# Kernel optimization log

Hardware: AMD Instinct MI355X
Metric: run time of the kernel (lower is better)

## Reference

```python
import jax, jax.numpy as jnp
import numpy as np
import math

LN_EPS = 1e-5

def layer_norm(x, g, b):
    m = x.mean(-1, keepdims=True)
    v = ((x - m) ** 2).mean(-1, keepdims=True)
    return (x - m) / jnp.sqrt(v + LN_EPS) * g + b

def bchw_to_bhwc(x):
    N, C, H, W = x.shape
    return x.transpose(0, 2, 3, 1).reshape(N, H * W, C)

def attw_matmul(weight, feature):
    # weight: [N,Q,K], feature: [N,C,FH,FW]; H=sqrt(Q), W=sqrt(K)
    N, Q, K = weight.shape
    _, C, FH, FW = feature.shape
    H, W = int(math.sqrt(Q)), int(math.sqrt(K))
    sH, sW = FH // H, FW // W
    # einsum('nij,ncjq->nciq', w, f).sum(3) == einsum over block-summed feature
    fs = feature.reshape(N, C, H, sH, W, sW).sum(axis=(3, 5)).reshape(N, C, H * W)  # [N,C,HW]
    r = jnp.einsum('nik,nck->nci', weight, fs)  # [N,C,HW]
    # broadcast-repeat each coarse cell back to its sH x sW block
    r = jnp.broadcast_to(r.reshape(N, C, H, 1, W, 1), (N, C, H, sH, W, sW))
    return r.reshape(N, C, H * sH, W * sW)

def reference(weight, feature, ln1_g, ln1_b, W1, b1, W2, b2, ln2_g, ln2_b, original_shape):
    residual = bchw_to_bhwc(feature)               # [N, FH*FW, C]
    x = bchw_to_bhwc(attw_matmul(weight, feature)) # [N, FH*FW, C]
    x = layer_norm(residual + x, ln1_g, ln1_b)
    residual = x
    h = jax.nn.gelu(x @ W1.T + b1, approximate=False)  # [N, T, dff]
    x = h @ W2.T + b2
    x = layer_norm(residual + x, ln2_g, ln2_b)
    return x

def setup_inputs() -> dict:
    key = jax.random.key(0)
    ks = jax.random.split(key, 8)
    N, C, FH, FW = 8, 256, 80, 80
    Q = K = 400
    hid, dff = 256, 1024
    s1 = 1.0 / math.sqrt(hid)
    s2 = 1.0 / math.sqrt(dff)
    return {
        "weight": jax.random.normal(ks[0], (N, Q, K), jnp.float32),
        "feature": jax.random.normal(ks[1], (N, C, FH, FW), jnp.float32),
        "ln1_g": jnp.ones((hid,), jnp.float32),
        "ln1_b": jnp.zeros((hid,), jnp.float32),
        "W1": jax.random.uniform(ks[2], (dff, hid), jnp.float32, -s1, s1),
        "b1": jax.random.uniform(ks[3], (dff,), jnp.float32, -s1, s1),
        "W2": jax.random.uniform(ks[4], (hid, dff), jnp.float32, -s2, s2),
        "b2": jax.random.uniform(ks[5], (hid,), jnp.float32, -s2, s2),
        "ln2_g": jnp.ones((hid,), jnp.float32),
        "ln2_b": jnp.zeros((hid,), jnp.float32),
        "original_shape": 80,
    }
```

## Files before the change

### kernel.cpp

```cpp
#include <hip/hip_runtime.h>
#include <hip/hip_bf16.h>
#include <math.h>

#define LN_EPS 1e-5f

typedef __attribute__((ext_vector_type(4))) float f4_t;
typedef __attribute__((ext_vector_type(8))) short bf8_t;

__device__ __forceinline__ unsigned short f2bf(float x) {
    unsigned u = __builtin_bit_cast(unsigned, x);
    unsigned r = (u + 0x7FFFu + ((u >> 16) & 1u)) >> 16;
    return (unsigned short)r;
}
__device__ __forceinline__ float bf2f(unsigned short u) {
    return __builtin_bit_cast(float, ((unsigned)u) << 16);
}
__device__ __forceinline__ float gelu_f(float x) {
    float z = x * 0.70710678f;
    float az = fabsf(z);
    float t = __builtin_amdgcn_rcpf(1.f + 0.3275911f * az);
    float y = t * (0.254829592f + t * (-0.284496736f + t * (1.421413741f +
              t * (-1.453152027f + t * 1.061405429f))));
    float e = 1.f - y * __expf(-az * az);
    return 0.5f * x * (1.f + copysignf(e, x));
}

__device__ __forceinline__ void light_barrier() {
    asm volatile("s_waitcnt lgkmcnt(0)" ::: "memory");
    __builtin_amdgcn_s_barrier();
}

__global__ __launch_bounds__(256) void pool_cvt_kernel(
    const float* __restrict__ feature, float* __restrict__ fs,
    const float* __restrict__ W1, const float* __restrict__ W2,
    bf8_t* __restrict__ W1f, bf8_t* __restrict__ W2f) {
    __shared__ float ftile[6400];
    int tid = threadIdx.x;
    if (blockIdx.x >= 2048) {
        int gid = (blockIdx.x - 2048) * 256 + tid;
        union { bf8_t v; unsigned short u[8]; } pk;
        if (gid < 32768) {
            int lane = gid & 63;
            int f = (gid >> 9) * 16 + (lane & 15);
            int k = ((gid >> 6) & 7) * 32 + (lane >> 4) * 8;
            const float* src = W1 + (size_t)f * 256 + k;
#pragma unroll
            for (int e = 0; e < 8; ++e) pk.u[e] = f2bf(src[e]);
            W1f[gid] = pk.v;
        } else {
            int g = gid - 32768;
            int lane = g & 63;
            int c = (g >> 11) * 16 + (lane & 15);
            int k = ((g >> 6) & 31) * 32 + (lane >> 4) * 8;
            const float* src = W2 + (size_t)c * 1024 + k;
#pragma unroll
            for (int e = 0; e < 8; ++e) pk.u[e] = f2bf(src[e]);
            W2f[g] = pk.v;
        }
        return;
    }
    int b = blockIdx.x;
    int n = b >> 8, c = b & 255;
    const float4* src = reinterpret_cast<const float4*>(feature + ((size_t)b) * 6400);
#pragma unroll
    for (int i = 0; i < 6; ++i) {
        int idx = i * 256 + tid;
        float4 v = src[idx];
        *reinterpret_cast<float4*>(&ftile[idx * 4]) = v;
    }
    if (tid < 64) {
        int idx = 1536 + tid;
        float4 v = src[idx];
        *reinterpret_cast<float4*>(&ftile[idx * 4]) = v;
    }
    __syncthreads();
    float* dst = fs + (size_t)n * 400 * 256 + c;
#pragma unroll
    for (int pass = 0; pass < 2; ++pass) {
        int k = pass * 256 + tid;
        if (k < 400) {
            int h = k / 20, w = k % 20;
            const float* p = &ftile[(h * 4) * 80 + w * 4];
            float s = 0.f;
#pragma unroll
            for (int dh = 0; dh < 4; ++dh)
                s += p[dh * 80 + 0] + p[dh * 80 + 1] + p[dh * 80 + 2] + p[dh * 80 + 3];
            dst[(size_t)k * 256] = s;
        }
    }
}

__global__ __launch_bounds__(256) void att_kernel(const float* __restrict__ wgt,
                                                  const float* __restrict__ fs,
                                                  float* __restrict__ r) {
    __shared__ float fsl[64][256];
    __shared__ float wl[8][64];
    int b = blockIdx.x;
    int n = b / 50, i0 = (b % 50) * 8;
    int tid = threadIdx.x;
    const float* wbase = wgt + (size_t)n * 400 * 400;
    const float* fsbase = fs + (size_t)n * 400 * 256;
    float acc[8] = {0.f, 0.f, 0.f, 0.f, 0.f, 0.f, 0.f, 0.f};
    for (int k0 = 0; k0 < 400; k0 += 64) {
        int kn = (k0 + 64 <= 400) ? 64 : (400 - k0);
        for (int kk = 0; kk < kn; ++kk)
            fsl[kk][tid] = fsbase[(size_t)(k0 + kk) * 256 + tid];
#pragma unroll
        for (int pass = 0; pass < 2; ++pass) {
            int idx = pass * 256 + tid;
            int ii = idx >> 6, kk = idx & 63;
            if (kk < kn)
                wl[ii][kk] = wbase[(size_t)(i0 + ii) * 400 + k0 + kk];
        }
        __syncthreads();
        for (int kk = 0; kk < kn; ++kk) {
            float f = fsl[kk][tid];
#pragma unroll
            for (int ii = 0; ii < 8; ++ii) acc[ii] += wl[ii][kk] * f;
        }
        __syncthreads();
    }
#pragma unroll
    for (int ii = 0; ii < 8; ++ii)
        r[((size_t)n * 400 + i0 + ii) * 256 + tid] = acc[ii];
}

__global__ __launch_bounds__(256, 2) void main_kernel(
    const float* __restrict__ feat, const float* __restrict__ r,
    const float* __restrict__ ln1g, const float* __restrict__ ln1b,
    const bf8_t* __restrict__ W1f, const float* __restrict__ b1,
    const bf8_t* __restrict__ W2f, const float* __restrict__ b2,
    const float* __restrict__ ln2g, const float* __restrict__ ln2b,
    float* __restrict__ out) {
    __shared__ unsigned short xt[64 * 256];
    __shared__ unsigned short ht[2][32 * 128];
    __shared__ float psum[4][64], psq[4][64];
    __shared__ float stat[2][64];

    int bid = blockIdx.x;
    int n = bid / 100;
    int p0 = (bid % 100) * 64;
    int tid = threadIdx.x;
    int lane = tid & 63;
    int q = tid >> 6;
    int t = lane;
    int p = p0 + t;
    int iatt = ((p / 80) >> 2) * 20 + ((p % 80) >> 2);

    const float* fbase = feat + ((size_t)(n * 256 + q * 64)) * 6400 + p;
    const float* rrow = r + ((size_t)(n * 400 + iatt)) * 256 + q * 64;
    float s1 = 0.f, s2 = 0.f;
#pragma unroll
    for (int jj = 0; jj < 8; ++jj) {
        union { bf8_t v; unsigned short u[8]; } pk;
#pragma unroll
        for (int e = 0; e < 8; ++e) {
            int j = jj * 8 + e;
            float v = fbase[(size_t)j * 6400] + rrow[j];
            s1 += v;
            s2 += v * v;
            pk.u[e] = f2bf(v);
        }
        int byte = t * 512 + ((q * 128 + jj * 16) ^ ((t & 7) << 4));
        *reinterpret_cast<bf8_t*>(reinterpret_cast<char*>(xt) + byte) = pk.v;
    }
    psum[q][t] = s1;
    psq[q][t] = s2;
    light_barrier();
    if (tid < 64) {
        float a = psum[0][tid] + psum[1][tid] + psum[2][tid] + psum[3][tid];
        float b = psq[0][tid] + psq[1][tid] + psq[2][tid] + psq[3][tid];
        float mu = a * (1.f / 256.f);
        float var = b * (1.f / 256.f) - mu * mu;
        stat[0][tid] = mu;
        stat[1][tid] = rsqrtf(var + LN_EPS);
    }
    light_barrier();
    float mu = stat[0][t], rs = stat[1][t];
#pragma unroll
    for (int jj = 0; jj < 8; ++jj) {
        int byte = t * 512 + ((q * 128 + jj * 16) ^ ((t & 7) << 4));
        union { bf8_t v; unsigned short u[8]; } pk;
        pk.v = *reinterpret_cast<const bf8_t*>(reinterpret_cast<const char*>(xt) + byte);
#pragma unroll
        for (int e = 0; e < 8; ++e) {
            int c = q * 64 + jj * 8 + e;
            float v = bf2f(pk.u[e]);
            pk.u[e] = f2bf((v - mu) * rs * ln1g[c] + ln1b[c]);
        }
        *reinterpret_cast<bf8_t*>(reinterpret_cast<char*>(xt) + byte) = pk.v;
    }
    light_barrier();

    int lm = lane & 15, lk = lane >> 4;
    const char* xtb = reinterpret_cast<const char*>(xt);

    f4_t oacc[16];
#pragma unroll
    for (int i = 0; i < 16; ++i) oacc[i] = (f4_t){0.f, 0.f, 0.f, 0.f};

    bf8_t bfr0[8];
    {
        const bf8_t* w1p = W1f + ((size_t)(0 * 8 + 2 * q) * 8) * 64 + lane;
#pragma unroll
        for (int kb = 0; kb < 4; ++kb) {
            bfr0[kb * 2 + 0] = w1p[(0 * 8 + kb) * 64];
            bfr0[kb * 2 + 1] = w1p[(1 * 8 + kb) * 64];
        }
    }

    for (int fc = 0; fc < 8; ++fc) {
        const bf8_t* w1p = W1f + ((size_t)(fc * 8 + 2 * q) * 8) * 64 + lane;
        f4_t hacc[8];
#pragma unroll
        for (int i = 0; i < 8; ++i) hacc[i] = (f4_t){0.f, 0.f, 0.f, 0.f};
#pragma unroll
        for (int kbh = 0; kbh < 2; ++kbh) {
            bf8_t bfr[8];
            if (kbh == 0) {
#pragma unroll
                for (int i = 0; i < 8; ++i) bfr[i] = bfr0[i];
            } else {
#pragma unroll
                for (int kb = 0; kb < 4; ++kb) {
                    bfr[kb * 2 + 0] = w1p[(0 * 8 + 4 + kb) * 64];
                    bfr[kb * 2 + 1] = w1p[(1 * 8 + 4 + kb) * 64];
                }
            }
#pragma unroll
            for (int kb = 0; kb < 4; ++kb) {
                int kbb = kbh * 4 + kb;
#pragma unroll
                for (int hh = 0; hh < 2; ++hh) {
#pragma unroll
                    for (int m = 0; m < 2; ++m) {
                        int row = hh * 32 + m * 16 + lm;
                        bf8_t a = *reinterpret_cast<const bf8_t*>(
                            xtb + row * 512 + ((kbb * 64 + lk * 16) ^ ((row & 7) << 4)));
                        hacc[hh * 4 + m * 2 + 0] = __builtin_amdgcn_mfma_f32_16x16x32_bf16(a, bfr[kb * 2 + 0], hacc[hh * 4 + m * 2 + 0], 0, 0, 0);
                        hacc[hh * 4 + m * 2 + 1] = __builtin_amdgcn_mfma_f32_16x16x32_bf16(a, bfr[kb * 2 + 1], hacc[hh * 4 + m * 2 + 1], 0, 0, 0);
                    }
                }
            }
        }
        const bf8_t* w2p = W2f + ((size_t)(q * 4) * 32 + fc * 4) * 64 + lane;
        bf8_t b2rA[8];
#pragma unroll
        for (int kb = 0; kb < 4; ++kb) {
            b2rA[kb * 2 + 0] = w2p[(0 * 32 + kb) * 64];
            b2rA[kb * 2 + 1] = w2p[(1 * 32 + kb) * 64];
        }
#pragma unroll
        for (int hh = 0; hh < 2; ++hh) {
            char* htc = reinterpret_cast<char*>(ht[hh]);
#pragma unroll
            for (int ftl = 0; ftl < 2; ++ftl) {
                int fl = (2 * q + ftl) * 16 + lm;
                float bias = b1[fc * 128 + fl];
#pragma unroll
                for (int m = 0; m < 2; ++m) {
#pragma unroll
                    for (int j = 0; j < 4; ++j) {
                        int row = m * 16 + lk * 4 + j;
                        float gv = gelu_f(hacc[hh * 4 + m * 2 + ftl][j] + bias);
                        *reinterpret_cast<unsigned short*>(
                            htc + row * 256 + ((fl * 2) ^ ((row & 7) << 4))) = f2bf(gv);
                    }
                }
            }
        }
        light_barrier();
        bf8_t b2rB[8];
#pragma unroll
        for (int kb = 0; kb < 4; ++kb) {
            b2rB[kb * 2 + 0] = w2p[(2 * 32 + kb) * 64];
            b2rB[kb * 2 + 1] = w2p[(3 * 32 + kb) * 64];
        }
        if (fc < 7) {
            const bf8_t* w1n = W1f + ((size_t)((fc + 1) * 8 + 2 * q) * 8) * 64 + lane;
#pragma unroll
            for (int kb = 0; kb < 4; ++kb) {
                bfr0[kb * 2 + 0] = w1n[(0 * 8 + kb) * 64];
                bfr0[kb * 2 + 1] = w1n[(1 * 8 + kb) * 64];
            }
        }
#pragma unroll
        for (int hh = 0; hh < 2; ++hh) {
            const char* htc = reinterpret_cast<const char*>(ht[hh]);
#pragma unroll
            for (int kb = 0; kb < 4; ++kb) {
#pragma unroll
                for (int m = 0; m < 2; ++m) {
                    int row = m * 16 + lm;
                    bf8_t a = *reinterpret_cast<const bf8_t*>(
                        htc + row * 256 + ((kb * 64 + lk * 16) ^ ((row & 7) << 4)));
                    oacc[hh * 8 + m * 4 + 0] = __builtin_amdgcn_mfma_f32_16x16x32_bf16(a, b2rA[kb * 2 + 0], oacc[hh * 8 + m * 4 + 0], 0, 0, 0);
                    oacc[hh * 8 + m * 4 + 1] = __builtin_amdgcn_mfma_f32_16x16x32_bf16(a, b2rA[kb * 2 + 1], oacc[hh * 8 + m * 4 + 1], 0, 0, 0);
                    oacc[hh * 8 + m * 4 + 2] = __builtin_amdgcn_mfma_f32_16x16x32_bf16(a, b2rB[kb * 2 + 0], oacc[hh * 8 + m * 4 + 2], 0, 0, 0);
                    oacc[hh * 8 + m * 4 + 3] = __builtin_amdgcn_mfma_f32_16x16x32_bf16(a, b2rB[kb * 2 + 1], oacc[hh * 8 + m * 4 + 3], 0, 0, 0);
                }
            }
        }
        light_barrier();
    }

    float b2l[4];
#pragma unroll
    for (int cl = 0; cl < 4; ++cl) b2l[cl] = b2[(q * 4 + cl) * 16 + lm];
#pragma unroll
    for (int hh = 0; hh < 2; ++hh) {
#pragma unroll
        for (int m = 0; m < 2; ++m) {
#pragma unroll
            for (int j = 0; j < 4; ++j) {
                int row = hh * 32 + m * 16 + lk * 4 + j;
                float s = 0.f, ss = 0.f;
#pragma unroll
                for (int cl = 0; cl < 4; ++cl) {
                    int c = (q * 4 + cl) * 16 + lm;
                    float res = bf2f(*reinterpret_cast<const unsigned short*>(
                        xtb + row * 512 + ((c * 2) ^ ((row & 7) << 4))));
                    float v = oacc[hh * 8 + m * 4 + cl][j] + b2l[cl] + res;
                    oacc[hh * 8 + m * 4 + cl][j] = v;
                    s += v;
                    ss += v * v;
                }
#pragma unroll
                for (int d = 1; d < 16; d <<= 1) {
                    s += __shfl_xor(s, d, 64);
                    ss += __shfl_xor(ss, d, 64);
                }
                if (lm == 0) { psum[q][row] = s; psq[q][row] = ss; }
            }
        }
    }
    light_barrier();
    if (tid < 64) {
        float a = psum[0][tid] + psum[1][tid] + psum[2][tid] + psum[3][tid];
        float b = psq[0][tid] + psq[1][tid] + psq[2][tid] + psq[3][tid];
        float mu2 = a * (1.f / 256.f);
        float var = b * (1.f / 256.f) - mu2 * mu2;
        stat[0][tid] = mu2;
        stat[1][tid] = rsqrtf(var + LN_EPS);
    }
    light_barrier();
    float g2[4], be2[4];
#pragma unroll
    for (int cl = 0; cl < 4; ++cl) {
        int c = (q * 4 + cl) * 16 + lm;
        g2[cl] = ln2g[c];
        be2[cl] = ln2b[c];
    }
    float* obase = out + ((size_t)(n * 6400 + p0)) * 256;
#pragma unroll
    for (int hh = 0; hh < 2; ++hh) {
#pragma unroll
        for (int m = 0; m < 2; ++m) {
#pragma unroll
            for (int j = 0; j < 4; ++j) {
                int row = hh * 32 + m * 16 + lk * 4 + j;
                float mu2 = stat[0][row], r2 = stat[1][row];
#pragma unroll
                for (int cl = 0; cl < 4; ++cl) {
                    int c = (q * 4 + cl) * 16 + lm;
                    obase[(size_t)row * 256 + c] =
                        (oacc[hh * 8 + m * 4 + cl][j] - mu2) * r2 * g2[cl] + be2[cl];
                }
            }
        }
    }
}

extern "C" void kernel_launch(void* const* d_in, const int* in_sizes, int n_in,
                              void* d_out, int out_size, void* d_ws, size_t ws_size,
                              hipStream_t stream) {
    const float* weight = (const float*)d_in[0];
    const float* feature = (const float*)d_in[1];
    const float* ln1g = (const float*)d_in[2];
    const float* ln1b = (const float*)d_in[3];
    const float* W1 = (const float*)d_in[4];
    const float* b1 = (const float*)d_in[5];
    const float* W2 = (const float*)d_in[6];
    const float* b2 = (const float*)d_in[7];
    const float* ln2g = (const float*)d_in[8];
    const float* ln2b = (const float*)d_in[9];
    float* outp = (float*)d_out;

    float* fs = (float*)d_ws;
    float* rbuf = fs + 819200;
    bf8_t* W1f = (bf8_t*)(rbuf + 819200);
    bf8_t* W2f = W1f + 32768;

    pool_cvt_kernel<<<2304, 256, 0, stream>>>(feature, fs, W1, W2, W1f, W2f);
    att_kernel<<<400, 256, 0, stream>>>(weight, fs, rbuf);
    main_kernel<<<800, 256, 0, stream>>>(feature, rbuf, ln1g, ln1b, W1f, b1,
                                         W2f, b2, ln2g, ln2b, outp);
}
```

Before: 154.6 us.

## Split main kernel work across eight waves per block instead of four

The fused LN/MLP/LN kernel now launches 512 threads per block, so each wave owns half as many channels, hidden features and output column tiles. Per-thread accumulators and weight fragments halve, which lowers register pressure and allows more resident waves per CU to hide memory and MFMA latency. The cost is that every wave still reads the full A fragments from LDS, so LDS read traffic for both GEMMs doubles. The LayerNorm partial-sum reductions are widened to eight groups.

```diff
diff --git a/kernel.cpp b/kernel.cpp
--- a/kernel.cpp
+++ b/kernel.cpp
@@ -125,7 +125,7 @@
         r[((size_t)n * 400 + i0 + ii) * 256 + tid] = acc[ii];
 }
 
-__global__ __launch_bounds__(256, 2) void main_kernel(
+__global__ __launch_bounds__(512, 2) void main_kernel(
     const float* __restrict__ feat, const float* __restrict__ r,
     const float* __restrict__ ln1g, const float* __restrict__ ln1b,
     const bf8_t* __restrict__ W1f, const float* __restrict__ b1,
@@ -134,7 +134,7 @@
     float* __restrict__ out) {
     __shared__ unsigned short xt[64 * 256];
     __shared__ unsigned short ht[2][32 * 128];
-    __shared__ float psum[4][64], psq[4][64];
+    __shared__ float psum[8][64], psq[8][64];
     __shared__ float stat[2][64];
 
     int bid = blockIdx.x;
@@ -147,11 +147,11 @@
     int p = p0 + t;
     int iatt = ((p / 80) >> 2) * 20 + ((p % 80) >> 2);
 
-    const float* fbase = feat + ((size_t)(n * 256 + q * 64)) * 6400 + p;
-    const float* rrow = r + ((size_t)(n * 400 + iatt)) * 256 + q * 64;
+    const float* fbase = feat + ((size_t)(n * 256 + q * 32)) * 6400 + p;
+    const float* rrow = r + ((size_t)(n * 400 + iatt)) * 256 + q * 32;
     float s1 = 0.f, s2 = 0.f;
 #pragma unroll
-    for (int jj = 0; jj < 8; ++jj) {
+    for (int jj = 0; jj < 4; ++jj) {
         union { bf8_t v; unsigned short u[8]; } pk;
 #pragma unroll
         for (int e = 0; e < 8; ++e) {
@@ -161,15 +161,16 @@
             s2 += v * v;
             pk.u[e] = f2bf(v);
         }
-        int byte = t * 512 + ((q * 128 + jj * 16) ^ ((t & 7) << 4));
+        int byte = t * 512 + ((q * 64 + jj * 16) ^ ((t & 7) << 4));
         *reinterpret_cast<bf8_t*>(reinterpret_cast<char*>(xt) + byte) = pk.v;
     }
     psum[q][t] = s1;
     psq[q][t] = s2;
     light_barrier();
     if (tid < 64) {
-        float a = psum[0][tid] + psum[1][tid] + psum[2][tid] + psum[3][tid];
-        float b = psq[0][tid] + psq[1][tid] + psq[2][tid] + psq[3][tid];
+        float a = 0.f, b = 0.f;
+#pragma unroll
+        for (int gg = 0; gg < 8; ++gg) { a += psum[gg][tid]; b += psq[gg][tid]; }
         float mu = a * (1.f / 256.f);
         float var = b * (1.f / 256.f) - mu * mu;
         stat[0][tid] = mu;
@@ -178,13 +179,13 @@
     light_barrier();
     float mu = stat[0][t], rs = stat[1][t];
 #pragma unroll
-    for (int jj = 0; jj < 8; ++jj) {
-        int byte = t * 512 + ((q * 128 + jj * 16) ^ ((t & 7) << 4));
+    for (int jj = 0; jj < 4; ++jj) {
+        int byte = t * 512 + ((q * 64 + jj * 16) ^ ((t & 7) << 4));
         union { bf8_t v; unsigned short u[8]; } pk;
         pk.v = *reinterpret_cast<const bf8_t*>(reinterpret_cast<const char*>(xt) + byte);
 #pragma unroll
         for (int e = 0; e < 8; ++e) {
-            int c = q * 64 + jj * 8 + e;
+            int c = q * 32 + jj * 8 + e;
             float v = bf2f(pk.u[e]);
             pk.u[e] = f2bf((v - mu) * rs * ln1g[c] + ln1b[c]);
         }
@@ -195,74 +196,54 @@
     int lm = lane & 15, lk = lane >> 4;
     const char* xtb = reinterpret_cast<const char*>(xt);
 
-    f4_t oacc[16];
-#pragma unroll
-    for (int i = 0; i < 16; ++i) oacc[i] = (f4_t){0.f, 0.f, 0.f, 0.f};
+    f4_t oacc[8];
+#pragma unroll
+    for (int i = 0; i < 8; ++i) oacc[i] = (f4_t){0.f, 0.f, 0.f, 0.f};
 
     bf8_t bfr0[8];
     {
-        const bf8_t* w1p = W1f + ((size_t)(0 * 8 + 2 * q) * 8) * 64 + lane;
+        const bf8_t* w1p = W1f + ((size_t)q * 8) * 64 + lane;
+#pragma unroll
+        for (int kb = 0; kb < 8; ++kb) bfr0[kb] = w1p[kb * 64];
+    }
+
+    for (int fc = 0; fc < 8; ++fc) {
+        f4_t hacc[4];
+#pragma unroll
+        for (int i = 0; i < 4; ++i) hacc[i] = (f4_t){0.f, 0.f, 0.f, 0.f};
+#pragma unroll
+        for (int kb = 0; kb < 8; ++kb) {
+#pragma unroll
+            for (int hh = 0; hh < 2; ++hh) {
+#pragma unroll
+                for (int m = 0; m < 2; ++m) {
+                    int row = hh * 32 + m * 16 + lm;
+                    bf8_t a = *reinterpret_cast<const bf8_t*>(
+                        xtb + row * 512 + ((kb * 64 + lk * 16) ^ ((row & 7) << 4)));
+                    hacc[hh * 2 + m] = __builtin_amdgcn_mfma_f32_16x16x32_bf16(a, bfr0[kb], hacc[hh * 2 + m], 0, 0, 0);
+                }
+            }
+        }
+        const bf8_t* w2pA = W2f + ((size_t)(2 * q) * 32 + fc * 4) * 64 + lane;
+        const bf8_t* w2pB = W2f + ((size_t)(2 * q + 1) * 32 + fc * 4) * 64 + lane;
+        bf8_t b2r[8];
 #pragma unroll
         for (int kb = 0; kb < 4; ++kb) {
-            bfr0[kb * 2 + 0] = w1p[(0 * 8 + kb) * 64];
-            bfr0[kb * 2 + 1] = w1p[(1 * 8 + kb) * 64];
-        }
-    }
-
-    for (int fc = 0; fc < 8; ++fc) {
-        const bf8_t* w1p = W1f + ((size_t)(fc * 8 + 2 * q) * 8) * 64 + lane;
-        f4_t hacc[8];
-#pragma unroll
-        for (int i = 0; i < 8; ++i) hacc[i] = (f4_t){0.f, 0.f, 0.f, 0.f};
-#pragma unroll
-        for (int kbh = 0; kbh < 2; ++kbh) {
-            bf8_t bfr[8];
-            if (kbh == 0) {
-#pragma unroll
-                for (int i = 0; i < 8; ++i) bfr[i] = bfr0[i];
-            } else {
-#pragma unroll
-                for (int kb = 0; kb < 4; ++kb) {
-                    bfr[kb * 2 + 0] = w1p[(0 * 8 + 4 + kb) * 64];
-                    bfr[kb * 2 + 1] = w1p[(1 * 8 + 4 + kb) * 64];
-                }
-            }
-#pragma unroll
-            for (int kb = 0; kb < 4; ++kb) {
-                int kbb = kbh * 4 + kb;
-#pragma unroll
-                for (int hh = 0; hh < 2; ++hh) {
-#pragma unroll
-                    for (int m = 0; m < 2; ++m) {
-                        int row = hh * 32 + m * 16 + lm;
-                        bf8_t a = *reinterpret_cast<const bf8_t*>(
-                            xtb + row * 512 + ((kbb * 64 + lk * 16) ^ ((row & 7) << 4)));
-                        hacc[hh * 4 + m * 2 + 0] = __builtin_amdgcn_mfma_f32_16x16x32_bf16(a, bfr[kb * 2 + 0], hacc[hh * 4 + m * 2 + 0], 0, 0, 0);
-                        hacc[hh * 4 + m * 2 + 1] = __builtin_amdgcn_mfma_f32_16x16x32_bf16(a, bfr[kb * 2 + 1], hacc[hh * 4 + m * 2 + 1], 0, 0, 0);
-                    }
-                }
-            }
-        }
-        const bf8_t* w2p = W2f + ((size_t)(q * 4) * 32 + fc * 4) * 64 + lane;
-        bf8_t b2rA[8];
-#pragma unroll
-        for (int kb = 0; kb < 4; ++kb) {
-            b2rA[kb * 2 + 0] = w2p[(0 * 32 + kb) * 64];
-            b2rA[kb * 2 + 1] = w2p[(1 * 32 + kb) * 64];
-        }
-#pragma unroll
-        for (int hh = 0; hh < 2; ++hh) {
-            char* htc = reinterpret_cast<char*>(ht[hh]);
-#pragma unroll
-            for (int ftl = 0; ftl < 2; ++ftl) {
-                int fl = (2 * q + ftl) * 16 + lm;
-                float bias = b1[fc * 128 + fl];
+            b2r[kb * 2 + 0] = w2pA[kb * 64];
+            b2r[kb * 2 + 1] = w2pB[kb * 64];
+        }
+        {
+            int fl = q * 16 + lm;
+            float bias = b1[fc * 128 + fl];
+#pragma unroll
+            for (int hh = 0; hh < 2; ++hh) {
+                char* htc = reinterpret_cast<char*>(ht[hh]);
 #pragma unroll
                 for (int m = 0; m < 2; ++m) {
 #pragma unroll
                     for (int j = 0; j < 4; ++j) {
                         int row = m * 16 + lk * 4 + j;
-                        float gv = gelu_f(hacc[hh * 4 + m * 2 + ftl][j] + bias);
+                        float gv = gelu_f(hacc[hh * 2 + m][j] + bias);
                         *reinterpret_cast<unsigned short*>(
                             htc + row * 256 + ((fl * 2) ^ ((row & 7) << 4))) = f2bf(gv);
                     }
@@ -270,19 +251,10 @@
             }
         }
         light_barrier();
-        bf8_t b2rB[8];
-#pragma unroll
-        for (int kb = 0; kb < 4; ++kb) {
-            b2rB[kb * 2 + 0] = w2p[(2 * 32 + kb) * 64];
-            b2rB[kb * 2 + 1] = w2p[(3 * 32 + kb) * 64];
-        }
         if (fc < 7) {
-            const bf8_t* w1n = W1f + ((size_t)((fc + 1) * 8 + 2 * q) * 8) * 64 + lane;
-#pragma unroll
-            for (int kb = 0; kb < 4; ++kb) {
-                bfr0[kb * 2 + 0] = w1n[(0 * 8 + kb) * 64];
-                bfr0[kb * 2 + 1] = w1n[(1 * 8 + kb) * 64];
-            }
+            const bf8_t* w1n = W1f + ((size_t)((fc + 1) * 8 + q) * 8) * 64 + lane;
+#pragma unroll
+            for (int kb = 0; kb < 8; ++kb) bfr0[kb] = w1n[kb * 64];
         }
 #pragma unroll
         for (int hh = 0; hh < 2; ++hh) {
@@ -294,19 +266,17 @@
                     int row = m * 16 + lm;
                     bf8_t a = *reinterpret_cast<const bf8_t*>(
                         htc + row * 256 + ((kb * 64 + lk * 16) ^ ((row & 7) << 4)));
-                    oacc[hh * 8 + m * 4 + 0] = __builtin_amdgcn_mfma_f32_16x16x32_bf16(a, b2rA[kb * 2 + 0], oacc[hh * 8 + m * 4 + 0], 0, 0, 0);
-                    oacc[hh * 8 + m * 4 + 1] = __builtin_amdgcn_mfma_f32_16x16x32_bf16(a, b2rA[kb * 2 + 1], oacc[hh * 8 + m * 4 + 1], 0, 0, 0);
-                    oacc[hh * 8 + m * 4 + 2] = __builtin_amdgcn_mfma_f32_16x16x32_bf16(a, b2rB[kb * 2 + 0], oacc[hh * 8 + m * 4 + 2], 0, 0, 0);
-                    oacc[hh * 8 + m * 4 + 3] = __builtin_amdgcn_mfma_f32_16x16x32_bf16(a, b2rB[kb * 2 + 1], oacc[hh * 8 + m * 4 + 3], 0, 0, 0);
+                    oacc[hh * 4 + m * 2 + 0] = __builtin_amdgcn_mfma_f32_16x16x32_bf16(a, b2r[kb * 2 + 0], oacc[hh * 4 + m * 2 + 0], 0, 0, 0);
+                    oacc[hh * 4 + m * 2 + 1] = __builtin_amdgcn_mfma_f32_16x16x32_bf16(a, b2r[kb * 2 + 1], oacc[hh * 4 + m * 2 + 1], 0, 0, 0);
                 }
             }
         }
         light_barrier();
     }
 
-    float b2l[4];
-#pragma unroll
-    for (int cl = 0; cl < 4; ++cl) b2l[cl] = b2[(q * 4 + cl) * 16 + lm];
+    float b2l[2];
+#pragma unroll
+    for (int cl = 0; cl < 2; ++cl) b2l[cl] = b2[(2 * q + cl) * 16 + lm];
 #pragma unroll
     for (int hh = 0; hh < 2; ++hh) {
 #pragma unroll
@@ -316,12 +286,12 @@
                 int row = hh * 32 + m * 16 + lk * 4 + j;
                 float s = 0.f, ss = 0.f;
 #pragma unroll
-                for (int cl = 0; cl < 4; ++cl) {
-                    int c = (q * 4 + cl) * 16 + lm;
+                for (int cl = 0; cl < 2; ++cl) {
+                    int c = (2 * q + cl) * 16 + lm;
                     float res = bf2f(*reinterpret_cast<const unsigned short*>(
                         xtb + row * 512 + ((c * 2) ^ ((row & 7) << 4))));
-                    float v = oacc[hh * 8 + m * 4 + cl][j] + b2l[cl] + res;
-                    oacc[hh * 8 + m * 4 + cl][j] = v;
+                    float v = oacc[hh * 4 + m * 2 + cl][j] + b2l[cl] + res;
+                    oacc[hh * 4 + m * 2 + cl][j] = v;
                     s += v;
                     ss += v * v;
                 }
@@ -336,18 +306,19 @@
     }
     light_barrier();
     if (tid < 64) {
-        float a = psum[0][tid] + psum[1][tid] + psum[2][tid] + psum[3][tid];
-        float b = psq[0][tid] + psq[1][tid] + psq[2][tid] + psq[3][tid];
+        float a = 0.f, b = 0.f;
+#pragma unroll
+        for (int gg = 0; gg < 8; ++gg) { a += psum[gg][tid]; b += psq[gg][tid]; }
         float mu2 = a * (1.f / 256.f);
         float var = b * (1.f / 256.f) - mu2 * mu2;
         stat[0][tid] = mu2;
         stat[1][tid] = rsqrtf(var + LN_EPS);
     }
     light_barrier();
-    float g2[4], be2[4];
-#pragma unroll
-    for (int cl = 0; cl < 4; ++cl) {
-        int c = (q * 4 + cl) * 16 + lm;
+    float g2[2], be2[2];
+#pragma unroll
+    for (int cl = 0; cl < 2; ++cl) {
+        int c = (2 * q + cl) * 16 + lm;
         g2[cl] = ln2g[c];
         be2[cl] = ln2b[c];
     }
@@ -361,10 +332,10 @@
                 int row = hh * 32 + m * 16 + lk * 4 + j;
                 float mu2 = stat[0][row], r2 = stat[1][row];
 #pragma unroll
-                for (int cl = 0; cl < 4; ++cl) {
-                    int c = (q * 4 + cl) * 16 + lm;
+                for (int cl = 0; cl < 2; ++cl) {
+                    int c = (2 * q + cl) * 16 + lm;
                     obase[(size_t)row * 256 + c] =
-                        (oacc[hh * 8 + m * 4 + cl][j] - mu2) * r2 * g2[cl] + be2[cl];
+                        (oacc[hh * 4 + m * 2 + cl][j] - mu2) * r2 * g2[cl] + be2[cl];
                 }
             }
         }
@@ -393,6 +364,6 @@
 
     pool_cvt_kernel<<<2304, 256, 0, stream>>>(feature, fs, W1, W2, W1f, W2f);
     att_kernel<<<400, 256, 0, stream>>>(weight, fs, rbuf);
-    main_kernel<<<800, 256, 0, stream>>>(feature, rbuf, ln1g, ln1b, W1f, b1,
+    main_kernel<<<800, 512, 0, stream>>>(feature, rbuf, ln1g, ln1b, W1f, b1,
                                          W2f, b2, ln2g, ln2b, outp);
 }
```

Result: slower. 198.4 us (+28.3%).

## Rewrite attention-weight matmul with bf16 MFMA and re-tiled blocks

Applied to the files above, without the earlier changes.

Replaces the scalar FP32 FMA loop in att_kernel with bf16 MFMA 16x16x32 instructions. Each block now computes a 16-row by 128-channel tile, staging feature sums into shared memory as bf16 with float4 loads. The grid shape stays the same. This cuts FP32 ALU work and shared-memory traffic, but rounding weights and block sums to bf16 lowers precision of the residual path before layernorm.

```diff
diff --git a/kernel.cpp b/kernel.cpp
--- a/kernel.cpp
+++ b/kernel.cpp
@@ -93,36 +93,64 @@
 __global__ __launch_bounds__(256) void att_kernel(const float* __restrict__ wgt,
                                                   const float* __restrict__ fs,
                                                   float* __restrict__ r) {
-    __shared__ float fsl[64][256];
-    __shared__ float wl[8][64];
+    __shared__ unsigned short fsl[32 * 128];
     int b = blockIdx.x;
-    int n = b / 50, i0 = (b % 50) * 8;
+    int n = b / 50;
+    int rem = b % 50;
+    int i0 = (rem >> 1) * 16;
+    int cb = (rem & 1) * 128;
     int tid = threadIdx.x;
-    const float* wbase = wgt + (size_t)n * 400 * 400;
-    const float* fsbase = fs + (size_t)n * 400 * 256;
-    float acc[8] = {0.f, 0.f, 0.f, 0.f, 0.f, 0.f, 0.f, 0.f};
-    for (int k0 = 0; k0 < 400; k0 += 64) {
-        int kn = (k0 + 64 <= 400) ? 64 : (400 - k0);
-        for (int kk = 0; kk < kn; ++kk)
-            fsl[kk][tid] = fsbase[(size_t)(k0 + kk) * 256 + tid];
-#pragma unroll
-        for (int pass = 0; pass < 2; ++pass) {
-            int idx = pass * 256 + tid;
-            int ii = idx >> 6, kk = idx & 63;
-            if (kk < kn)
-                wl[ii][kk] = wbase[(size_t)(i0 + ii) * 400 + k0 + kk];
-        }
-        __syncthreads();
-        for (int kk = 0; kk < kn; ++kk) {
-            float f = fsl[kk][tid];
-#pragma unroll
-            for (int ii = 0; ii < 8; ++ii) acc[ii] += wl[ii][kk] * f;
-        }
-        __syncthreads();
-    }
-#pragma unroll
-    for (int ii = 0; ii < 8; ++ii)
-        r[((size_t)n * 400 + i0 + ii) * 256 + tid] = acc[ii];
+    int lane = tid & 63;
+    int q = tid >> 6;
+    int lm = lane & 15, lk = lane >> 4;
+    const float* wbase = wgt + (size_t)n * 400 * 400 + (size_t)(i0 + lm) * 400;
+    const float* fsb = fs + (size_t)n * 400 * 256 + cb;
+    f4_t acc[2];
+    acc[0] = (f4_t){0.f, 0.f, 0.f, 0.f};
+    acc[1] = (f4_t){0.f, 0.f, 0.f, 0.f};
+    for (int kc = 0; kc < 13; ++kc) {
+        int k0 = kc * 32;
+#pragma unroll
+        for (int r4 = 0; r4 < 4; ++r4) {
+            int idx = r4 * 256 + tid;
+            int k = idx >> 5;
+            int c4 = (idx & 31) * 4;
+            float4 v;
+            if (k0 + k < 400)
+                v = *reinterpret_cast<const float4*>(fsb + (size_t)(k0 + k) * 256 + c4);
+            else
+                v = make_float4(0.f, 0.f, 0.f, 0.f);
+            unsigned short* d = &fsl[k * 128 + c4];
+            d[0] = f2bf(v.x); d[1] = f2bf(v.y); d[2] = f2bf(v.z); d[3] = f2bf(v.w);
+        }
+        union { bf8_t v; unsigned short u[8]; } af;
+        int ka = k0 + lk * 8;
+        if (ka < 400) {
+#pragma unroll
+            for (int e = 0; e < 8; ++e) af.u[e] = f2bf(wbase[ka + e]);
+        } else {
+#pragma unroll
+            for (int e = 0; e < 8; ++e) af.u[e] = 0;
+        }
+        light_barrier();
+#pragma unroll
+        for (int ntl = 0; ntl < 2; ++ntl) {
+            int c = (q * 2 + ntl) * 16 + lm;
+            union { bf8_t v; unsigned short u[8]; } bf;
+#pragma unroll
+            for (int e = 0; e < 8; ++e) bf.u[e] = fsl[(lk * 8 + e) * 128 + c];
+            acc[ntl] = __builtin_amdgcn_mfma_f32_16x16x32_bf16(af.v, bf.v, acc[ntl], 0, 0, 0);
+        }
+        light_barrier();
+    }
+    float* rb = r + ((size_t)n * 400 + i0) * 256 + cb;
+#pragma unroll
+    for (int ntl = 0; ntl < 2; ++ntl) {
+        int c = (q * 2 + ntl) * 16 + lm;
+#pragma unroll
+        for (int j = 0; j < 4; ++j)
+            rb[(size_t)(lk * 4 + j) * 256 + c] = acc[ntl][j];
+    }
 }
 
 __global__ __launch_bounds__(256, 2) void main_kernel(
```

After: 146.5 us. 5.3% less time.
